# Kernel tuning notes

Measured on AMD Instinct MI355X. Metric: run time of the kernel, lower is better.

The kernel has to match this reference:

```python
import jax, jax.numpy as jnp
import numpy as np

EPS = 1e-5

def _batchnorm(x, gamma, beta):
    # training-mode BatchNorm1d: biased variance over the batch axis
    mean = jnp.mean(x, axis=0)
    var = jnp.mean(jnp.square(x - mean), axis=0)
    return (x - mean) * jax.lax.rsqrt(var + EPS) * gamma + beta

def setup_inputs() -> dict:
    key = jax.random.key(0)
    ks = jax.random.split(key, 20)
    N, E, T = 100000, 400000, 1000000
    ATOM, BOND, ANGLE = 128, 128, 64
    s = 0.05
    return {
        "vertex_feat": jax.random.normal(ks[0], (N, ATOM), jnp.float32),
        "edge_feat": jax.random.normal(ks[1], (E, BOND), jnp.float32),
        "angle_feat": jax.random.normal(ks[2], (T, ANGLE), jnp.float32),
        "edge_index": jax.random.randint(ks[3], (2, E), 0, N),
        "k_idx": jax.random.randint(ks[4], (T,), 0, E),   # b_i: bond indices
        "j_idx": jax.random.randint(ks[5], (T,), 0, N),   # a: center atom indices
        "i_idx": jax.random.randint(ks[6], (T,), 0, N),   # b_j: indexes vertex rows per source code
        "w_core_src": jax.random.normal(ks[7], (BOND, ATOM), jnp.float32) * s,
        "w_core_dst": jax.random.normal(ks[8], (BOND, ATOM), jnp.float32) * s,
        "w_core_bond": jax.random.normal(ks[9], (BOND, BOND), jnp.float32) * s,
        "w_core_angle": jax.random.normal(ks[10], (BOND, ANGLE), jnp.float32) * s,
        "w_gate_src": jax.random.normal(ks[11], (BOND, ATOM), jnp.float32) * s,
        "w_gate_dst": jax.random.normal(ks[12], (BOND, ATOM), jnp.float32) * s,
        "w_gate_bond": jax.random.normal(ks[13], (BOND, BOND), jnp.float32) * s,
        "w_gate_angle": jax.random.normal(ks[14], (BOND, ANGLE), jnp.float32) * s,
        "bn_core_gamma": jnp.ones((BOND,), jnp.float32),
        "bn_core_beta": jnp.zeros((BOND,), jnp.float32),
        "bn_gate_gamma": jnp.ones((BOND,), jnp.float32),
        "bn_gate_beta": jnp.zeros((BOND,), jnp.float32),
        "w_out": jax.random.normal(ks[15], (BOND, BOND), jnp.float32) * s,
    }

def _branch(vertex_feat, edge_feat, angle_feat, k_idx, j_idx, i_idx, ws, wd, wb, wa):
    # reverse_scatter chain == gather-add:
    # out[t] = (angle @ wa.T)[t] + (v @ ws.T)[j_idx[t]] + (e @ wb.T)[k_idx[t]] + (v @ wd.T)[i_idx[t]]
    center = vertex_feat @ ws.T            # [N, bond]
    bond_i = edge_feat @ wb.T              # [E, bond]
    bond_j = vertex_feat @ wd.T            # [N, bond]
    angles = angle_feat @ wa.T             # [T, bond]
    return angles + center[j_idx] + bond_i[k_idx] + bond_j[i_idx]

def reference(vertex_feat, edge_feat, angle_feat, edge_index, k_idx, j_idx, i_idx,
              w_core_src, w_core_dst, w_core_bond, w_core_angle,
              w_gate_src, w_gate_dst, w_gate_bond, w_gate_angle,
              bn_core_gamma, bn_core_beta, bn_gate_gamma, bn_gate_beta, w_out):
    E = edge_feat.shape[0]
    core = _branch(vertex_feat, edge_feat, angle_feat, k_idx, j_idx, i_idx,
                   w_core_src, w_core_dst, w_core_bond, w_core_angle)   # [T, bond]
    gate = _branch(vertex_feat, edge_feat, angle_feat, k_idx, j_idx, i_idx,
                   w_gate_src, w_gate_dst, w_gate_bond, w_gate_angle)   # [T, bond]
    core = jax.nn.silu(_batchnorm(core, bn_core_gamma, bn_core_beta))
    gate = jax.nn.sigmoid(_batchnorm(gate, bn_gate_gamma, bn_gate_beta))
    update = core * gate                                                # [T, bond]
    new_bond = jax.ops.segment_sum(update, k_idx, num_segments=E)       # [E, bond]
    new_bond = new_bond @ w_out.T
    return new_bond + edge_feat
```

## Files before the change

kernel.cpp:

```cpp
#include <hip/hip_runtime.h>
#include <hip/hip_bf16.h>

typedef unsigned short u16;
typedef unsigned int u32;
typedef __attribute__((ext_vector_type(8))) short bf8;
typedef __attribute__((ext_vector_type(4))) float f32x4;

__device__ __forceinline__ float bf2f(u16 u) {
    u32 v = ((u32)u) << 16;
    float f;
    __builtin_memcpy(&f, &v, 4);
    return f;
}
__device__ __forceinline__ u16 f2bf(float f) {
    u32 v;
    __builtin_memcpy(&v, &f, 4);
    u32 r = (v + 0x7fffu + ((v >> 16) & 1u)) >> 16;
    return (u16)r;
}
__device__ __forceinline__ u32 pk2(float a, float b) {
    return (u32)f2bf(a) | ((u32)f2bf(b) << 16);
}
__device__ __forceinline__ void unpack4(uint2 u, float* f) {
    f[0] = bf2f((u16)(u.x & 0xffffu));
    f[1] = bf2f((u16)(u.x >> 16));
    f[2] = bf2f((u16)(u.y & 0xffffu));
    f[3] = bf2f((u16)(u.y >> 16));
}

#define BM 128
#define BN 128
#define BK 64
#define LSTR 72

__global__ void detect_dtype(const u16* __restrict__ v, int* __restrict__ flag)
{
    __shared__ int red[256];
    int tid = threadIdx.x;
    int cnt = 0;
    for (int i = tid; i < 8192; i += 256) {
        u16 u = v[2 * i];
        int e = (u >> 7) & 0xFF;
        cnt += (e >= 160) ? 1 : 0;
    }
    red[tid] = cnt;
    __syncthreads();
    for (int s = 128; s > 0; s >>= 1) {
        if (tid < s) red[tid] += red[tid + s];
        __syncthreads();
    }
    if (tid == 0) flag[0] = (red[0] > 400) ? 1 : 0;
}

__global__ __launch_bounds__(256)
void gemm_bt(const void* __restrict__ Av, const u16* __restrict__ W,
             u16* __restrict__ C, const int* __restrict__ flag,
             int M, int K, int Ncols)
{
    __shared__ u16 As[BM][LSTR];
    __shared__ u16 Ws[BN][LSTR];
    const bool isf32 = flag[0] != 0;
    const int tid = threadIdx.x;
    const int m0 = blockIdx.x * BM;
    const int n0 = blockIdx.y * BN;
    const int wave = tid >> 6, lane = tid & 63;
    const int l16 = lane & 15, quad = lane >> 4;
    const int wrow = (wave >> 1) * 64, wcol = (wave & 1) * 64;

    f32x4 acc[4][4];
    for (int mi = 0; mi < 4; ++mi)
        for (int ni = 0; ni < 4; ++ni)
            for (int r = 0; r < 4; ++r) acc[mi][ni][r] = 0.f;

    for (int kk = 0; kk < K; kk += BK) {
        for (int it = 0; it < 4; ++it) {
            int c = tid + it * 256;
            int row = c >> 3, col8 = (c & 7) * 8;
            uint4 v = make_uint4(0, 0, 0, 0);
            int gr = m0 + row;
            if (gr < M) {
                if (!isf32) {
                    v = *(const uint4*)((const u16*)Av + (size_t)gr * K + (kk + col8));
                } else {
                    const float* Af = (const float*)Av + (size_t)gr * K + (kk + col8);
                    float4 x = *(const float4*)Af;
                    float4 y = *(const float4*)(Af + 4);
                    v = make_uint4(pk2(x.x, x.y), pk2(x.z, x.w), pk2(y.x, y.y), pk2(y.z, y.w));
                }
            }
            *(uint4*)(&As[row][col8]) = v;
        }
        for (int it = 0; it < 4; ++it) {
            int c = tid + it * 256;
            int row = c >> 3, col8 = (c & 7) * 8;
            uint4 v = *(const uint4*)(W + (size_t)(n0 + row) * K + (kk + col8));
            *(uint4*)(&Ws[row][col8]) = v;
        }
        __syncthreads();
        for (int ko = 0; ko < BK; ko += 32) {
            bf8 af[4], bw[4];
            for (int mi = 0; mi < 4; ++mi)
                af[mi] = *(const bf8*)(&As[wrow + mi * 16 + l16][ko + quad * 8]);
            for (int ni = 0; ni < 4; ++ni)
                bw[ni] = *(const bf8*)(&Ws[wcol + ni * 16 + l16][ko + quad * 8]);
            for (int mi = 0; mi < 4; ++mi)
                for (int ni = 0; ni < 4; ++ni)
                    acc[mi][ni] = __builtin_amdgcn_mfma_f32_16x16x32_bf16(
                        af[mi], bw[ni], acc[mi][ni], 0, 0, 0);
        }
        __syncthreads();
    }
    for (int mi = 0; mi < 4; ++mi) {
        int rbase = m0 + wrow + mi * 16 + quad * 4;
        for (int r = 0; r < 4; ++r) {
            int row = rbase + r;
            if (row >= M) continue;
            for (int ni = 0; ni < 4; ++ni) {
                int col = n0 + wcol + ni * 16 + l16;
                C[(size_t)row * Ncols + col] = f2bf(acc[mi][ni][r]);
            }
        }
    }
}

__global__ __launch_bounds__(256)
void gemm_out(const float* __restrict__ Aacc, const void* __restrict__ Wv_,
              const void* __restrict__ Edgev, void* __restrict__ Outv,
              const int* __restrict__ flag, int M)
{
    __shared__ u16 As[BM][LSTR];
    __shared__ u16 Ws[BN][LSTR];
    const bool isf32 = flag[0] != 0;
    const int tid = threadIdx.x;
    const int m0 = blockIdx.x * BM;
    const int wave = tid >> 6, lane = tid & 63;
    const int l16 = lane & 15, quad = lane >> 4;
    const int wrow = (wave >> 1) * 64, wcol = (wave & 1) * 64;

    f32x4 acc[4][4];
    for (int mi = 0; mi < 4; ++mi)
        for (int ni = 0; ni < 4; ++ni)
            for (int r = 0; r < 4; ++r) acc[mi][ni][r] = 0.f;

    for (int kk = 0; kk < 128; kk += BK) {
        for (int it = 0; it < 4; ++it) {
            int c = tid + it * 256;
            int row = c >> 3, col8 = (c & 7) * 8;
            int gr = m0 + row;
            uint4 v = make_uint4(0, 0, 0, 0);
            if (gr < M) {
                const float* src = Aacc + (size_t)gr * 128 + kk + col8;
                v = make_uint4(pk2(src[0], src[1]), pk2(src[2], src[3]),
                               pk2(src[4], src[5]), pk2(src[6], src[7]));
            }
            *(uint4*)(&As[row][col8]) = v;
        }
        for (int it = 0; it < 4; ++it) {
            int c = tid + it * 256;
            int row = c >> 3, col8 = (c & 7) * 8;
            uint4 v;
            if (!isf32) {
                v = *(const uint4*)((const u16*)Wv_ + (size_t)row * 128 + (kk + col8));
            } else {
                const float* Wf = (const float*)Wv_ + (size_t)row * 128 + (kk + col8);
                float4 x = *(const float4*)Wf;
                float4 y = *(const float4*)(Wf + 4);
                v = make_uint4(pk2(x.x, x.y), pk2(x.z, x.w), pk2(y.x, y.y), pk2(y.z, y.w));
            }
            *(uint4*)(&Ws[row][col8]) = v;
        }
        __syncthreads();
        for (int ko = 0; ko < BK; ko += 32) {
            bf8 af[4], bw[4];
            for (int mi = 0; mi < 4; ++mi)
                af[mi] = *(const bf8*)(&As[wrow + mi * 16 + l16][ko + quad * 8]);
            for (int ni = 0; ni < 4; ++ni)
                bw[ni] = *(const bf8*)(&Ws[wcol + ni * 16 + l16][ko + quad * 8]);
            for (int mi = 0; mi < 4; ++mi)
                for (int ni = 0; ni < 4; ++ni)
                    acc[mi][ni] = __builtin_amdgcn_mfma_f32_16x16x32_bf16(
                        af[mi], bw[ni], acc[mi][ni], 0, 0, 0);
        }
        __syncthreads();
    }
    for (int mi = 0; mi < 4; ++mi) {
        int rbase = m0 + wrow + mi * 16 + quad * 4;
        for (int r = 0; r < 4; ++r) {
            int row = rbase + r;
            if (row >= M) continue;
            for (int ni = 0; ni < 4; ++ni) {
                int col = wcol + ni * 16 + l16;
                size_t idx = (size_t)row * 128 + col;
                float e = isf32 ? ((const float*)Edgev)[idx] : bf2f(((const u16*)Edgev)[idx]);
                float v = acc[mi][ni][r] + e;
                if (isf32) ((float*)Outv)[idx] = v;
                else       ((u16*)Outv)[idx] = f2bf(v);
            }
        }
    }
}

__global__ __launch_bounds__(256)
void gather_stats(u16* __restrict__ CG, const u16* __restrict__ Vout,
                  const u16* __restrict__ Eout,
                  const int* __restrict__ jidx, const int* __restrict__ kidx,
                  const int* __restrict__ iidx, float* __restrict__ stats, int T)
{
    const int tid = threadIdx.x;
    const int q = tid & 63;
    const int wv = tid >> 6;
    const int p = q * 4;
    float sum[4] = {0.f, 0.f, 0.f, 0.f};
    float ssq[4] = {0.f, 0.f, 0.f, 0.f};
    for (long t = (long)blockIdx.x * 4 + wv; t < T; t += (long)gridDim.x * 4) {
        int j = jidx[t], k = kidx[t], i = iidx[t];
        uint2 ua = *(const uint2*)(CG + t * 256 + p);
        uint2 uj = *(const uint2*)(Vout + (size_t)j * 512 + p);
        uint2 uk = *(const uint2*)(Eout + (size_t)k * 256 + p);
        uint2 ui = *(const uint2*)(Vout + (size_t)i * 512 + 256 + p);
        float fa[4], fj[4], fk[4], fi[4];
        unpack4(ua, fa); unpack4(uj, fj); unpack4(uk, fk); unpack4(ui, fi);
        float v[4];
        for (int x = 0; x < 4; ++x) {
            v[x] = fa[x] + fj[x] + fk[x] + fi[x];
            sum[x] += v[x];
            ssq[x] += v[x] * v[x];
        }
        uint2 o;
        o.x = pk2(v[0], v[1]);
        o.y = pk2(v[2], v[3]);
        *(uint2*)(CG + t * 256 + p) = o;
    }
    __shared__ float red[512];
    red[tid] = 0.f;
    red[tid + 256] = 0.f;
    __syncthreads();
    for (int x = 0; x < 4; ++x) {
        atomicAdd(&red[p + x], sum[x]);
        atomicAdd(&red[256 + p + x], ssq[x]);
    }
    __syncthreads();
    atomicAdd(&stats[tid], red[tid]);
    atomicAdd(&stats[tid + 256], red[tid + 256]);
}

__global__ void bn_finalize(const float* __restrict__ stats,
                            const void* __restrict__ gc, const void* __restrict__ bc,
                            const void* __restrict__ gg, const void* __restrict__ bg,
                            float* __restrict__ ab, const int* __restrict__ flag,
                            float invT)
{
    const bool isf32 = flag[0] != 0;
    int p = threadIdx.x;
    float mean = stats[p] * invT;
    float var = stats[256 + p] * invT - mean * mean;
    const void* gsrc = (p < 128) ? gc : gg;
    const void* bsrc = (p < 128) ? bc : bg;
    int pi = p & 127;
    float g = isf32 ? ((const float*)gsrc)[pi] : bf2f(((const u16*)gsrc)[pi]);
    float b = isf32 ? ((const float*)bsrc)[pi] : bf2f(((const u16*)bsrc)[pi]);
    float a = g * rsqrtf(var + 1e-5f);
    ab[p] = a;
    ab[256 + p] = b - mean * a;
}


__global__ __launch_bounds__(256)
void hist_k(const int* __restrict__ kidx, int* __restrict__ cnt, int T)
{
    for (int t = blockIdx.x * 256 + threadIdx.x; t < T; t += gridDim.x * 256)
        atomicAdd(&cnt[kidx[t]], 1);
}

#define SCHUNK 2048

__global__ __launch_bounds__(256)
void scan_blocks(const int* __restrict__ cnt, int* __restrict__ bsum, int E)
{
    __shared__ int red[256];
    int b = blockIdx.x, t = threadIdx.x;
    int base = b * SCHUNK + t * 8;
    int s = 0;
    for (int i = 0; i < 8; ++i) {
        int idx = base + i;
        s += (idx < E) ? cnt[idx] : 0;
    }
    red[t] = s;
    __syncthreads();
    for (int st = 128; st > 0; st >>= 1) {
        if (t < st) red[t] += red[t + st];
        __syncthreads();
    }
    if (t == 0) bsum[b] = red[0];
}

__global__ void scan_partials(int* __restrict__ bsum, int NB,
                              int* __restrict__ offs, int E, int T)
{
    __shared__ int sh[256];
    int t = threadIdx.x;
    int v = (t < NB) ? bsum[t] : 0;
    sh[t] = v;
    __syncthreads();
    for (int d = 1; d < 256; d <<= 1) {
        int x = (t >= d) ? sh[t - d] : 0;
        __syncthreads();
        sh[t] += x;
        __syncthreads();
    }
    if (t < NB) bsum[t] = sh[t] - v;
    if (t == 0) offs[E] = T;
}

__global__ __launch_bounds__(256)
void scan_chunks(const int* __restrict__ cnt, const int* __restrict__ bsum,
                 int* __restrict__ offs, int E)
{
    __shared__ int sh[256];
    int b = blockIdx.x, t = threadIdx.x;
    int base = b * SCHUNK + t * 8;
    int loc[8];
    int s = 0;
    for (int i = 0; i < 8; ++i) {
        int idx = base + i;
        loc[i] = (idx < E) ? cnt[idx] : 0;
    }
    for (int i = 0; i < 8; ++i) { int v = loc[i]; loc[i] = s; s += v; }
    sh[t] = s;
    __syncthreads();
    for (int d = 1; d < 256; d <<= 1) {
        int x = (t >= d) ? sh[t - d] : 0;
        __syncthreads();
        sh[t] += x;
        __syncthreads();
    }
    int ex = sh[t] - s;
    int off = bsum[b] + ex;
    for (int i = 0; i < 8; ++i) {
        int idx = base + i;
        if (idx < E) offs[idx] = off + loc[i];
    }
}

__global__ __launch_bounds__(256)
void fill_k(const int* __restrict__ kidx, const int* __restrict__ offs,
            int* __restrict__ cur, int* __restrict__ blist, int T)
{
    for (int t = blockIdx.x * 256 + threadIdx.x; t < T; t += gridDim.x * 256) {
        int k = kidx[t];
        int pos = offs[k] + atomicAdd(&cur[k], 1);
        blist[pos] = t;
    }
}

__global__ __launch_bounds__(256)
void seg_update(const u16* __restrict__ CG, const float* __restrict__ ab,
                const int* __restrict__ offs, const int* __restrict__ blist,
                float* __restrict__ acc, int E)
{
    const int tid = threadIdx.x;
    const int q = tid & 63;
    const int wv = tid >> 6;
    const int f = q * 2;
    const float ac0 = ab[f], ac1 = ab[f + 1];
    const float ag0 = ab[128 + f], ag1 = ab[128 + f + 1];
    const float bc0 = ab[256 + f], bc1 = ab[256 + f + 1];
    const float bg0 = ab[384 + f], bg1 = ab[384 + f + 1];
    for (int e = blockIdx.x * 4 + wv; e < E; e += gridDim.x * 4) {
        int s = offs[e], en = offs[e + 1];
        float u0 = 0.f, u1 = 0.f;
        for (int idx = s; idx < en; ++idx) {
            int t = blist[idx];
            u32 c2 = *(const u32*)(CG + (size_t)t * 256 + f);
            u32 g2 = *(const u32*)(CG + (size_t)t * 256 + 128 + f);
            float c0 = bf2f((u16)(c2 & 0xffffu)) * ac0 + bc0;
            float c1 = bf2f((u16)(c2 >> 16)) * ac1 + bc1;
            float g0 = bf2f((u16)(g2 & 0xffffu)) * ag0 + bg0;
            float g1 = bf2f((u16)(g2 >> 16)) * ag1 + bg1;
            float s0 = 1.f / (1.f + __expf(-c0));
            float s1 = 1.f / (1.f + __expf(-c1));
            float t0 = 1.f / (1.f + __expf(-g0));
            float t1 = 1.f / (1.f + __expf(-g1));
            u0 += c0 * s0 * t0;
            u1 += c1 * s1 * t1;
        }
        *(float2*)(acc + (size_t)e * 128 + f) = make_float2(u0, u1);
    }
}

__device__ __forceinline__ u16 ld_bf(const void* p, size_t idx, bool isf32)
{
    return isf32 ? f2bf(((const float*)p)[idx]) : ((const u16*)p)[idx];
}

__global__ void pack_weights(const void* __restrict__ wcs, const void* __restrict__ wcd,
                             const void* __restrict__ wcb, const void* __restrict__ wca,
                             const void* __restrict__ wgs, const void* __restrict__ wgd,
                             const void* __restrict__ wgb, const void* __restrict__ wga,
                             u16* __restrict__ Wv, u16* __restrict__ We, u16* __restrict__ Wa,
                             const int* __restrict__ flag)
{
    const bool isf32 = flag[0] != 0;
    int tid = blockIdx.x * 256 + threadIdx.x;
    {
        int row = tid >> 7, col = tid & 127;
        const void* src = (row < 128) ? wcs : (row < 256) ? wgs : (row < 384) ? wcd : wgd;
        Wv[tid] = ld_bf(src, (size_t)(row & 127) * 128 + col, isf32);
    }
    if (tid < 256 * 128) {
        int row = tid >> 7, col = tid & 127;
        const void* src = (row < 128) ? wcb : wgb;
        We[tid] = ld_bf(src, (size_t)(row & 127) * 128 + col, isf32);
    }
    if (tid < 256 * 64) {
        int row = tid >> 6, col = tid & 63;
        const void* src = (row < 128) ? wca : wga;
        Wa[tid] = ld_bf(src, (size_t)(row & 127) * 64 + col, isf32);
    }
}

extern "C" void kernel_launch(void* const* d_in, const int* in_sizes, int n_in,
                              void* d_out, int out_size, void* d_ws, size_t ws_size,
                              hipStream_t stream)
{
    const void* vertex = d_in[0];
    const void* edge   = d_in[1];
    const void* angle  = d_in[2];
    const int* kidx = (const int*)d_in[4];
    const int* jidx = (const int*)d_in[5];
    const int* iidx = (const int*)d_in[6];

    const int N = in_sizes[0] / 128;
    const int E = in_sizes[1] / 128;
    const int T = in_sizes[2] / 64;

    char* p = (char*)d_ws;
    auto alloc = [&](size_t bytes) {
        char* r = p;
        p += (bytes + 255) & ~(size_t)255;
        return r;
    };
    u16* Wv = (u16*)alloc((size_t)512 * 128 * 2);
    u16* We = (u16*)alloc((size_t)256 * 128 * 2);
    u16* Wa = (u16*)alloc((size_t)256 * 64 * 2);
    float* stats = (float*)alloc(512 * 4);
    float* ab = (float*)alloc(512 * 4);
    int* flag = (int*)alloc(256);
    u16* Vout = (u16*)alloc((size_t)N * 512 * 2);
    u16* Eout = (u16*)alloc((size_t)E * 256 * 2);
    u16* CG   = (u16*)alloc((size_t)T * 256 * 2);
    float* acc = (float*)Vout;

    char* tail = (char*)acc + (size_t)E * 512;
    int* cnt   = (int*)tail;
    int* offs  = cnt + ((E + 63) & ~63);
    int* blist = offs + ((E + 1 + 63) & ~63);
    int* bsum  = blist + ((T + 63) & ~63);
    const int NB = (E + SCHUNK - 1) / SCHUNK;

    hipMemsetAsync(stats, 0, 512 * 4, stream);
    detect_dtype<<<1, 256, 0, stream>>>((const u16*)vertex, flag);
    pack_weights<<<256, 256, 0, stream>>>(d_in[7], d_in[8], d_in[9], d_in[10],
                                          d_in[11], d_in[12], d_in[13], d_in[14],
                                          Wv, We, Wa, flag);
    gemm_bt<<<dim3((N + 127) / 128, 4), 256, 0, stream>>>(vertex, Wv, Vout, flag, N, 128, 512);
    gemm_bt<<<dim3((E + 127) / 128, 2), 256, 0, stream>>>(edge, We, Eout, flag, E, 128, 256);
    gemm_bt<<<dim3((T + 127) / 128, 2), 256, 0, stream>>>(angle, Wa, CG, flag, T, 64, 256);
    gather_stats<<<2048, 256, 0, stream>>>(CG, Vout, Eout, jidx, kidx, iidx, stats, T);

    hipMemsetAsync(cnt, 0, (size_t)E * 4, stream);
    hist_k<<<2048, 256, 0, stream>>>(kidx, cnt, T);
    scan_blocks<<<NB, 256, 0, stream>>>(cnt, bsum, E);
    scan_partials<<<1, 256, 0, stream>>>(bsum, NB, offs, E, T);
    scan_chunks<<<NB, 256, 0, stream>>>(cnt, bsum, offs, E);
    hipMemsetAsync(cnt, 0, (size_t)E * 4, stream);
    fill_k<<<2048, 256, 0, stream>>>(kidx, offs, cnt, blist, T);

    bn_finalize<<<1, 256, 0, stream>>>(stats, d_in[15], d_in[16], d_in[17], d_in[18],
                                       ab, flag, 1.0f / (float)T);
    seg_update<<<2048, 256, 0, stream>>>(CG, ab, offs, blist, acc, E);
    gemm_out<<<dim3((E + 127) / 128, 1), 256, 0, stream>>>(acc, d_in[19], edge, d_out, flag, E);
}
```

Baseline: 1.902 ms.

## Fuse angle GEMM with gather-add and batch-norm statistics epilogue

Replaces the separate angle-feature GEMM and the gather_stats pass with a single kernel. Each tile's GEMM output is staged in shared memory, then the gathered vertex and edge projections are added, and per-channel sum and sum-of-squares are accumulated before CG is written once. This removes one full write and read of the T x 256 bf16 intermediate. Statistics now go into 64 partial slots to reduce atomic contention, and bn_finalize sums those slots. In exchange, each block's gather uses 2-element per-lane loads instead of 4, and the kernel uses more shared memory per block.

Result: no change. 1.909 ms (+0.4%).

```diff
diff --git a/kernel.cpp b/kernel.cpp
--- a/kernel.cpp
+++ b/kernel.cpp
@@ -124,6 +124,112 @@
 }
 
 __global__ __launch_bounds__(256)
+void gemm_angle_fused(const void* __restrict__ Av, const u16* __restrict__ Wa,
+                      const u16* __restrict__ Vout, const u16* __restrict__ Eout,
+                      const int* __restrict__ jidx, const int* __restrict__ kidx,
+                      const int* __restrict__ iidx,
+                      u16* __restrict__ CG, float* __restrict__ stats2,
+                      const int* __restrict__ flag, int T)
+{
+    __shared__ u16 sh[2 * BM * LSTR];
+    u16 (*As)[LSTR] = (u16(*)[LSTR])sh;
+    u16 (*Ws)[LSTR] = (u16(*)[LSTR])(sh + BM * LSTR);
+    const bool isf32 = flag[0] != 0;
+    const int tid = threadIdx.x;
+    const int m0 = blockIdx.x * BM;
+    const int h = blockIdx.y;
+    const int n0 = h * 128;
+    const int wave = tid >> 6, lane = tid & 63;
+    const int l16 = lane & 15, quad = lane >> 4;
+    const int wrow = (wave >> 1) * 64, wcol = (wave & 1) * 64;
+
+    f32x4 acc[4][4];
+    for (int mi = 0; mi < 4; ++mi)
+        for (int ni = 0; ni < 4; ++ni)
+            for (int r = 0; r < 4; ++r) acc[mi][ni][r] = 0.f;
+
+    for (int it = 0; it < 4; ++it) {
+        int c = tid + it * 256;
+        int row = c >> 3, col8 = (c & 7) * 8;
+        uint4 v = make_uint4(0, 0, 0, 0);
+        int gr = m0 + row;
+        if (gr < T) {
+            if (!isf32) {
+                v = *(const uint4*)((const u16*)Av + (size_t)gr * 64 + col8);
+            } else {
+                const float* Af = (const float*)Av + (size_t)gr * 64 + col8;
+                float4 x = *(const float4*)Af;
+                float4 y = *(const float4*)(Af + 4);
+                v = make_uint4(pk2(x.x, x.y), pk2(x.z, x.w), pk2(y.x, y.y), pk2(y.z, y.w));
+            }
+        }
+        *(uint4*)(&As[row][col8]) = v;
+    }
+    for (int it = 0; it < 4; ++it) {
+        int c = tid + it * 256;
+        int row = c >> 3, col8 = (c & 7) * 8;
+        uint4 v = *(const uint4*)(Wa + (size_t)(n0 + row) * 64 + col8);
+        *(uint4*)(&Ws[row][col8]) = v;
+    }
+    __syncthreads();
+    for (int ko = 0; ko < 64; ko += 32) {
+        bf8 af[4], bw[4];
+        for (int mi = 0; mi < 4; ++mi)
+            af[mi] = *(const bf8*)(&As[wrow + mi * 16 + l16][ko + quad * 8]);
+        for (int ni = 0; ni < 4; ++ni)
+            bw[ni] = *(const bf8*)(&Ws[wcol + ni * 16 + l16][ko + quad * 8]);
+        for (int mi = 0; mi < 4; ++mi)
+            for (int ni = 0; ni < 4; ++ni)
+                acc[mi][ni] = __builtin_amdgcn_mfma_f32_16x16x32_bf16(
+                    af[mi], bw[ni], acc[mi][ni], 0, 0, 0);
+    }
+    __syncthreads();
+
+    u16 (*Cs)[136] = (u16(*)[136])sh;
+    for (int mi = 0; mi < 4; ++mi) {
+        int rbase = wrow + mi * 16 + quad * 4;
+        for (int r = 0; r < 4; ++r)
+            for (int ni = 0; ni < 4; ++ni)
+                Cs[rbase + r][wcol + ni * 16 + l16] = f2bf(acc[mi][ni][r]);
+    }
+    __syncthreads();
+
+    const int q = lane;
+    const int p = q * 2;
+    float sum0 = 0.f, sum1 = 0.f, ssq0 = 0.f, ssq1 = 0.f;
+    for (int rr = wave; rr < 128; rr += 4) {
+        long t = (long)m0 + rr;
+        if (t >= T) break;
+        int j = jidx[t], k = kidx[t], i = iidx[t];
+        u32 ua = *(const u32*)(&Cs[rr][p]);
+        u32 uj = *(const u32*)(Vout + (size_t)j * 512 + n0 + p);
+        u32 uk = *(const u32*)(Eout + (size_t)k * 256 + n0 + p);
+        u32 ui = *(const u32*)(Vout + (size_t)i * 512 + 256 + n0 + p);
+        float v0 = bf2f((u16)(ua & 0xffffu)) + bf2f((u16)(uj & 0xffffu))
+                 + bf2f((u16)(uk & 0xffffu)) + bf2f((u16)(ui & 0xffffu));
+        float v1 = bf2f((u16)(ua >> 16)) + bf2f((u16)(uj >> 16))
+                 + bf2f((u16)(uk >> 16)) + bf2f((u16)(ui >> 16));
+        sum0 += v0; sum1 += v1;
+        ssq0 += v0 * v0; ssq1 += v1 * v1;
+        *(u32*)(CG + (size_t)t * 256 + n0 + p) = pk2(v0, v1);
+    }
+
+    __syncthreads();
+    float* red = (float*)sh;
+    red[wave * 128 + p] = sum0;
+    red[wave * 128 + p + 1] = sum1;
+    red[512 + wave * 128 + p] = ssq0;
+    red[512 + wave * 128 + p + 1] = ssq1;
+    __syncthreads();
+    {
+        int c = tid & 127, s = tid >> 7;
+        float v = red[s * 512 + c] + red[s * 512 + 128 + c]
+                + red[s * 512 + 256 + c] + red[s * 512 + 384 + c];
+        atomicAdd(&stats2[(size_t)(blockIdx.x & 63) * 512 + s * 256 + n0 + c], v);
+    }
+}
+
+__global__ __launch_bounds__(256)
 void gemm_out(const float* __restrict__ Aacc, const void* __restrict__ Wv_,
               const void* __restrict__ Edgev, void* __restrict__ Outv,
               const int* __restrict__ flag, int M)
@@ -200,51 +306,7 @@
     }
 }
 
-__global__ __launch_bounds__(256)
-void gather_stats(u16* __restrict__ CG, const u16* __restrict__ Vout,
-                  const u16* __restrict__ Eout,
-                  const int* __restrict__ jidx, const int* __restrict__ kidx,
-                  const int* __restrict__ iidx, float* __restrict__ stats, int T)
-{
-    const int tid = threadIdx.x;
-    const int q = tid & 63;
-    const int wv = tid >> 6;
-    const int p = q * 4;
-    float sum[4] = {0.f, 0.f, 0.f, 0.f};
-    float ssq[4] = {0.f, 0.f, 0.f, 0.f};
-    for (long t = (long)blockIdx.x * 4 + wv; t < T; t += (long)gridDim.x * 4) {
-        int j = jidx[t], k = kidx[t], i = iidx[t];
-        uint2 ua = *(const uint2*)(CG + t * 256 + p);
-        uint2 uj = *(const uint2*)(Vout + (size_t)j * 512 + p);
-        uint2 uk = *(const uint2*)(Eout + (size_t)k * 256 + p);
-        uint2 ui = *(const uint2*)(Vout + (size_t)i * 512 + 256 + p);
-        float fa[4], fj[4], fk[4], fi[4];
-        unpack4(ua, fa); unpack4(uj, fj); unpack4(uk, fk); unpack4(ui, fi);
-        float v[4];
-        for (int x = 0; x < 4; ++x) {
-            v[x] = fa[x] + fj[x] + fk[x] + fi[x];
-            sum[x] += v[x];
-            ssq[x] += v[x] * v[x];
-        }
-        uint2 o;
-        o.x = pk2(v[0], v[1]);
-        o.y = pk2(v[2], v[3]);
-        *(uint2*)(CG + t * 256 + p) = o;
-    }
-    __shared__ float red[512];
-    red[tid] = 0.f;
-    red[tid + 256] = 0.f;
-    __syncthreads();
-    for (int x = 0; x < 4; ++x) {
-        atomicAdd(&red[p + x], sum[x]);
-        atomicAdd(&red[256 + p + x], ssq[x]);
-    }
-    __syncthreads();
-    atomicAdd(&stats[tid], red[tid]);
-    atomicAdd(&stats[tid + 256], red[tid + 256]);
-}
-
-__global__ void bn_finalize(const float* __restrict__ stats,
+__global__ void bn_finalize(const float* __restrict__ stats2,
                             const void* __restrict__ gc, const void* __restrict__ bc,
                             const void* __restrict__ gg, const void* __restrict__ bg,
                             float* __restrict__ ab, const int* __restrict__ flag,
@@ -252,8 +314,13 @@
 {
     const bool isf32 = flag[0] != 0;
     int p = threadIdx.x;
-    float mean = stats[p] * invT;
-    float var = stats[256 + p] * invT - mean * mean;
+    float s = 0.f, q = 0.f;
+    for (int k = 0; k < 64; ++k) {
+        s += stats2[(size_t)k * 512 + p];
+        q += stats2[(size_t)k * 512 + 256 + p];
+    }
+    float mean = s * invT;
+    float var = q * invT - mean * mean;
     const void* gsrc = (p < 128) ? gc : gg;
     const void* bsrc = (p < 128) ? bc : bg;
     int pi = p & 127;
@@ -443,7 +510,7 @@
     u16* Wv = (u16*)alloc((size_t)512 * 128 * 2);
     u16* We = (u16*)alloc((size_t)256 * 128 * 2);
     u16* Wa = (u16*)alloc((size_t)256 * 64 * 2);
-    float* stats = (float*)alloc(512 * 4);
+    float* stats2 = (float*)alloc((size_t)64 * 512 * 4);
     float* ab = (float*)alloc(512 * 4);
     int* flag = (int*)alloc(256);
     u16* Vout = (u16*)alloc((size_t)N * 512 * 2);
@@ -458,15 +525,15 @@
     int* bsum  = blist + ((T + 63) & ~63);
     const int NB = (E + SCHUNK - 1) / SCHUNK;
 
-    hipMemsetAsync(stats, 0, 512 * 4, stream);
+    hipMemsetAsync(stats2, 0, (size_t)64 * 512 * 4, stream);
     detect_dtype<<<1, 256, 0, stream>>>((const u16*)vertex, flag);
     pack_weights<<<256, 256, 0, stream>>>(d_in[7], d_in[8], d_in[9], d_in[10],
                                           d_in[11], d_in[12], d_in[13], d_in[14],
                                           Wv, We, Wa, flag);
     gemm_bt<<<dim3((N + 127) / 128, 4), 256, 0, stream>>>(vertex, Wv, Vout, flag, N, 128, 512);
     gemm_bt<<<dim3((E + 127) / 128, 2), 256, 0, stream>>>(edge, We, Eout, flag, E, 128, 256);
-    gemm_bt<<<dim3((T + 127) / 128, 2), 256, 0, stream>>>(angle, Wa, CG, flag, T, 64, 256);
-    gather_stats<<<2048, 256, 0, stream>>>(CG, Vout, Eout, jidx, kidx, iidx, stats, T);
+    gemm_angle_fused<<<dim3((T + 127) / 128, 2), 256, 0, stream>>>(
+        angle, Wa, Vout, Eout, jidx, kidx, iidx, CG, stats2, flag, T);
 
     hipMemsetAsync(cnt, 0, (size_t)E * 4, stream);
     hist_k<<<2048, 256, 0, stream>>>(kidx, cnt, T);
@@ -476,7 +543,7 @@
     hipMemsetAsync(cnt, 0, (size_t)E * 4, stream);
     fill_k<<<2048, 256, 0, stream>>>(kidx, offs, cnt, blist, T);
 
-    bn_finalize<<<1, 256, 0, stream>>>(stats, d_in[15], d_in[16], d_in[17], d_in[18],
+    bn_finalize<<<1, 256, 0, stream>>>(stats2, d_in[15], d_in[16], d_in[17], d_in[18],
                                        ab, flag, 1.0f / (float)T);
     seg_update<<<2048, 256, 0, stream>>>(CG, ab, offs, blist, acc, E);
     gemm_out<<<dim3((E + 127) / 128, 1), 256, 0, stream>>>(acc, d_in[19], edge, d_out, flag, E);
```

## Fuse segment-sum update with output GEMM and swap GEMM grid axes

Applied to the files above, without the earlier changes.

Merges the segmented sum of the gated update and the final w_out projection into one kernel. Each block reduces 128 edge rows into shared memory as bf16, then runs MFMA against a pre-packed bf16 w_out read directly from global memory. This removes the fp32 intermediate accumulator round trip through HBM and one kernel launch. It also swaps the grid axes of gemm_bt so blocks sharing an A row-tile run adjacently, and adds nontemporal loads and stores on the streamed CG buffer. The cost is lower parallelism in the segment phase (fixed 32 rows per wave, one block per 128 edges) and an extra bf16 rounding of the summed update before the GEMM.

Result: slower. 2.015 ms (+5.9%).

```diff
diff --git a/kernel.cpp b/kernel.cpp
--- a/kernel.cpp
+++ b/kernel.cpp
@@ -4,6 +4,7 @@
 typedef unsigned short u16;
 typedef unsigned int u32;
 typedef __attribute__((ext_vector_type(8))) short bf8;
+typedef __attribute__((ext_vector_type(2))) unsigned int u32x2;
 typedef __attribute__((ext_vector_type(4))) float f32x4;
 
 __device__ __forceinline__ float bf2f(u16 u) {
@@ -20,12 +21,6 @@
 }
 __device__ __forceinline__ u32 pk2(float a, float b) {
     return (u32)f2bf(a) | ((u32)f2bf(b) << 16);
-}
-__device__ __forceinline__ void unpack4(uint2 u, float* f) {
-    f[0] = bf2f((u16)(u.x & 0xffffu));
-    f[1] = bf2f((u16)(u.x >> 16));
-    f[2] = bf2f((u16)(u.y & 0xffffu));
-    f[3] = bf2f((u16)(u.y >> 16));
 }
 
 #define BM 128
@@ -61,8 +56,8 @@
     __shared__ u16 Ws[BN][LSTR];
     const bool isf32 = flag[0] != 0;
     const int tid = threadIdx.x;
-    const int m0 = blockIdx.x * BM;
-    const int n0 = blockIdx.y * BN;
+    const int m0 = blockIdx.y * BM;
+    const int n0 = blockIdx.x * BN;
     const int wave = tid >> 6, lane = tid & 63;
     const int l16 = lane & 15, quad = lane >> 4;
     const int wrow = (wave >> 1) * 64, wcol = (wave & 1) * 64;
@@ -124,83 +119,6 @@
 }
 
 __global__ __launch_bounds__(256)
-void gemm_out(const float* __restrict__ Aacc, const void* __restrict__ Wv_,
-              const void* __restrict__ Edgev, void* __restrict__ Outv,
-              const int* __restrict__ flag, int M)
-{
-    __shared__ u16 As[BM][LSTR];
-    __shared__ u16 Ws[BN][LSTR];
-    const bool isf32 = flag[0] != 0;
-    const int tid = threadIdx.x;
-    const int m0 = blockIdx.x * BM;
-    const int wave = tid >> 6, lane = tid & 63;
-    const int l16 = lane & 15, quad = lane >> 4;
-    const int wrow = (wave >> 1) * 64, wcol = (wave & 1) * 64;
-
-    f32x4 acc[4][4];
-    for (int mi = 0; mi < 4; ++mi)
-        for (int ni = 0; ni < 4; ++ni)
-            for (int r = 0; r < 4; ++r) acc[mi][ni][r] = 0.f;
-
-    for (int kk = 0; kk < 128; kk += BK) {
-        for (int it = 0; it < 4; ++it) {
-            int c = tid + it * 256;
-            int row = c >> 3, col8 = (c & 7) * 8;
-            int gr = m0 + row;
-            uint4 v = make_uint4(0, 0, 0, 0);
-            if (gr < M) {
-                const float* src = Aacc + (size_t)gr * 128 + kk + col8;
-                v = make_uint4(pk2(src[0], src[1]), pk2(src[2], src[3]),
-                               pk2(src[4], src[5]), pk2(src[6], src[7]));
-            }
-            *(uint4*)(&As[row][col8]) = v;
-        }
-        for (int it = 0; it < 4; ++it) {
-            int c = tid + it * 256;
-            int row = c >> 3, col8 = (c & 7) * 8;
-            uint4 v;
-            if (!isf32) {
-                v = *(const uint4*)((const u16*)Wv_ + (size_t)row * 128 + (kk + col8));
-            } else {
-                const float* Wf = (const float*)Wv_ + (size_t)row * 128 + (kk + col8);
-                float4 x = *(const float4*)Wf;
-                float4 y = *(const float4*)(Wf + 4);
-                v = make_uint4(pk2(x.x, x.y), pk2(x.z, x.w), pk2(y.x, y.y), pk2(y.z, y.w));
-            }
-            *(uint4*)(&Ws[row][col8]) = v;
-        }
-        __syncthreads();
-        for (int ko = 0; ko < BK; ko += 32) {
-            bf8 af[4], bw[4];
-            for (int mi = 0; mi < 4; ++mi)
-                af[mi] = *(const bf8*)(&As[wrow + mi * 16 + l16][ko + quad * 8]);
-            for (int ni = 0; ni < 4; ++ni)
-                bw[ni] = *(const bf8*)(&Ws[wcol + ni * 16 + l16][ko + quad * 8]);
-            for (int mi = 0; mi < 4; ++mi)
-                for (int ni = 0; ni < 4; ++ni)
-                    acc[mi][ni] = __builtin_amdgcn_mfma_f32_16x16x32_bf16(
-                        af[mi], bw[ni], acc[mi][ni], 0, 0, 0);
-        }
-        __syncthreads();
-    }
-    for (int mi = 0; mi < 4; ++mi) {
-        int rbase = m0 + wrow + mi * 16 + quad * 4;
-        for (int r = 0; r < 4; ++r) {
-            int row = rbase + r;
-            if (row >= M) continue;
-            for (int ni = 0; ni < 4; ++ni) {
-                int col = wcol + ni * 16 + l16;
-                size_t idx = (size_t)row * 128 + col;
-                float e = isf32 ? ((const float*)Edgev)[idx] : bf2f(((const u16*)Edgev)[idx]);
-                float v = acc[mi][ni][r] + e;
-                if (isf32) ((float*)Outv)[idx] = v;
-                else       ((u16*)Outv)[idx] = f2bf(v);
-            }
-        }
-    }
-}
-
-__global__ __launch_bounds__(256)
 void gather_stats(u16* __restrict__ CG, const u16* __restrict__ Vout,
                   const u16* __restrict__ Eout,
                   const int* __restrict__ jidx, const int* __restrict__ kidx,
@@ -214,22 +132,27 @@
     float ssq[4] = {0.f, 0.f, 0.f, 0.f};
     for (long t = (long)blockIdx.x * 4 + wv; t < T; t += (long)gridDim.x * 4) {
         int j = jidx[t], k = kidx[t], i = iidx[t];
-        uint2 ua = *(const uint2*)(CG + t * 256 + p);
+        u32x2 ua = __builtin_nontemporal_load((const u32x2*)(CG + t * 256 + p));
         uint2 uj = *(const uint2*)(Vout + (size_t)j * 512 + p);
         uint2 uk = *(const uint2*)(Eout + (size_t)k * 256 + p);
         uint2 ui = *(const uint2*)(Vout + (size_t)i * 512 + 256 + p);
-        float fa[4], fj[4], fk[4], fi[4];
-        unpack4(ua, fa); unpack4(uj, fj); unpack4(uk, fk); unpack4(ui, fi);
         float v[4];
+        v[0] = bf2f((u16)(ua[0] & 0xffffu)) + bf2f((u16)(uj.x & 0xffffu))
+             + bf2f((u16)(uk.x & 0xffffu)) + bf2f((u16)(ui.x & 0xffffu));
+        v[1] = bf2f((u16)(ua[0] >> 16)) + bf2f((u16)(uj.x >> 16))
+             + bf2f((u16)(uk.x >> 16)) + bf2f((u16)(ui.x >> 16));
+        v[2] = bf2f((u16)(ua[1] & 0xffffu)) + bf2f((u16)(uj.y & 0xffffu))
+             + bf2f((u16)(uk.y & 0xffffu)) + bf2f((u16)(ui.y & 0xffffu));
+        v[3] = bf2f((u16)(ua[1] >> 16)) + bf2f((u16)(uj.y >> 16))
+             + bf2f((u16)(uk.y >> 16)) + bf2f((u16)(ui.y >> 16));
         for (int x = 0; x < 4; ++x) {
-            v[x] = fa[x] + fj[x] + fk[x] + fi[x];
             sum[x] += v[x];
             ssq[x] += v[x] * v[x];
         }
-        uint2 o;
-        o.x = pk2(v[0], v[1]);
-        o.y = pk2(v[2], v[3]);
-        *(uint2*)(CG + t * 256 + p) = o;
+        u32x2 o;
+        o[0] = pk2(v[0], v[1]);
+        o[1] = pk2(v[2], v[3]);
+        __builtin_nontemporal_store(o, (u32x2*)(CG + t * 256 + p));
     }
     __shared__ float red[512];
     red[tid] = 0.f;
@@ -354,37 +277,86 @@
 }
 
 __global__ __launch_bounds__(256)
-void seg_update(const u16* __restrict__ CG, const float* __restrict__ ab,
-                const int* __restrict__ offs, const int* __restrict__ blist,
-                float* __restrict__ acc, int E)
-{
+void seg_gemm_out(const u16* __restrict__ CG, const float* __restrict__ ab,
+                  const int* __restrict__ offs, const int* __restrict__ blist,
+                  const u16* __restrict__ Wo, const void* __restrict__ Edgev,
+                  void* __restrict__ Outv, const int* __restrict__ flag, int E)
+{
+    __shared__ u16 As[128][136];
+    const bool isf32 = flag[0] != 0;
     const int tid = threadIdx.x;
-    const int q = tid & 63;
-    const int wv = tid >> 6;
-    const int f = q * 2;
-    const float ac0 = ab[f], ac1 = ab[f + 1];
-    const float ag0 = ab[128 + f], ag1 = ab[128 + f + 1];
-    const float bc0 = ab[256 + f], bc1 = ab[256 + f + 1];
-    const float bg0 = ab[384 + f], bg1 = ab[384 + f + 1];
-    for (int e = blockIdx.x * 4 + wv; e < E; e += gridDim.x * 4) {
-        int s = offs[e], en = offs[e + 1];
-        float u0 = 0.f, u1 = 0.f;
-        for (int idx = s; idx < en; ++idx) {
-            int t = blist[idx];
-            u32 c2 = *(const u32*)(CG + (size_t)t * 256 + f);
-            u32 g2 = *(const u32*)(CG + (size_t)t * 256 + 128 + f);
-            float c0 = bf2f((u16)(c2 & 0xffffu)) * ac0 + bc0;
-            float c1 = bf2f((u16)(c2 >> 16)) * ac1 + bc1;
-            float g0 = bf2f((u16)(g2 & 0xffffu)) * ag0 + bg0;
-            float g1 = bf2f((u16)(g2 >> 16)) * ag1 + bg1;
-            float s0 = 1.f / (1.f + __expf(-c0));
-            float s1 = 1.f / (1.f + __expf(-c1));
-            float t0 = 1.f / (1.f + __expf(-g0));
-            float t1 = 1.f / (1.f + __expf(-g1));
-            u0 += c0 * s0 * t0;
-            u1 += c1 * s1 * t1;
-        }
-        *(float2*)(acc + (size_t)e * 128 + f) = make_float2(u0, u1);
+    const int wave = tid >> 6, lane = tid & 63;
+    const int m0 = blockIdx.x * 128;
+    const int f = lane * 2;
+
+    {
+        const float ac0 = ab[f], ac1 = ab[f + 1];
+        const float ag0 = ab[128 + f], ag1 = ab[128 + f + 1];
+        const float bc0 = ab[256 + f], bc1 = ab[256 + f + 1];
+        const float bg0 = ab[384 + f], bg1 = ab[384 + f + 1];
+        for (int i = 0; i < 32; ++i) {
+            int rl = wave * 32 + i;
+            int e = m0 + rl;
+            float u0 = 0.f, u1 = 0.f;
+            if (e < E) {
+                int s = offs[e], en = offs[e + 1];
+                for (int idx = s; idx < en; ++idx) {
+                    int t = blist[idx];
+                    u32 c2 = __builtin_nontemporal_load(
+                        (const u32*)(CG + (size_t)t * 256 + f));
+                    u32 g2 = __builtin_nontemporal_load(
+                        (const u32*)(CG + (size_t)t * 256 + 128 + f));
+                    float c0 = bf2f((u16)(c2 & 0xffffu)) * ac0 + bc0;
+                    float c1 = bf2f((u16)(c2 >> 16)) * ac1 + bc1;
+                    float g0 = bf2f((u16)(g2 & 0xffffu)) * ag0 + bg0;
+                    float g1 = bf2f((u16)(g2 >> 16)) * ag1 + bg1;
+                    float s0 = 1.f / (1.f + __expf(-c0));
+                    float s1 = 1.f / (1.f + __expf(-c1));
+                    float t0 = 1.f / (1.f + __expf(-g0));
+                    float t1 = 1.f / (1.f + __expf(-g1));
+                    u0 += c0 * s0 * t0;
+                    u1 += c1 * s1 * t1;
+                }
+            }
+            *(u32*)(&As[rl][f]) = pk2(u0, u1);
+        }
+    }
+    __syncthreads();
+
+    const int l16 = lane & 15, quad = lane >> 4;
+    const int wrow = (wave >> 1) * 64, wcol = (wave & 1) * 64;
+    f32x4 acc[4][4];
+    for (int mi = 0; mi < 4; ++mi)
+        for (int ni = 0; ni < 4; ++ni)
+            for (int r = 0; r < 4; ++r) acc[mi][ni][r] = 0.f;
+
+    for (int kk = 0; kk < 128; kk += 32) {
+        bf8 af[4], bw[4];
+        for (int mi = 0; mi < 4; ++mi)
+            af[mi] = *(const bf8*)(&As[wrow + mi * 16 + l16][kk + quad * 8]);
+        for (int ni = 0; ni < 4; ++ni)
+            bw[ni] = *(const bf8*)(Wo + (size_t)(wcol + ni * 16 + l16) * 128
+                                       + kk + quad * 8);
+        for (int mi = 0; mi < 4; ++mi)
+            for (int ni = 0; ni < 4; ++ni)
+                acc[mi][ni] = __builtin_amdgcn_mfma_f32_16x16x32_bf16(
+                    af[mi], bw[ni], acc[mi][ni], 0, 0, 0);
+    }
+
+    for (int mi = 0; mi < 4; ++mi) {
+        int rbase = m0 + wrow + mi * 16 + quad * 4;
+        for (int r = 0; r < 4; ++r) {
+            int row = rbase + r;
+            if (row >= E) continue;
+            for (int ni = 0; ni < 4; ++ni) {
+                int col = wcol + ni * 16 + l16;
+                size_t idx = (size_t)row * 128 + col;
+                float e = isf32 ? ((const float*)Edgev)[idx] : bf2f(((const u16*)Edgev)[idx]);
+                float v = acc[mi][ni][r] + e;
+                if (isf32) ((float*)Outv)[idx] = v;
+                else       ((u16*)Outv)[idx] = f2bf(v);
+            }
+        }
     }
 }
 
@@ -397,7 +369,9 @@
                              const void* __restrict__ wcb, const void* __restrict__ wca,
                              const void* __restrict__ wgs, const void* __restrict__ wgd,
                              const void* __restrict__ wgb, const void* __restrict__ wga,
-                             u16* __restrict__ Wv, u16* __restrict__ We, u16* __restrict__ Wa,
+                             const void* __restrict__ wout,
+                             u16* __restrict__ Wv, u16* __restrict__ We,
+                             u16* __restrict__ Wa, u16* __restrict__ Wo,
                              const int* __restrict__ flag)
 {
     const bool isf32 = flag[0] != 0;
@@ -416,6 +390,9 @@
         int row = tid >> 6, col = tid & 63;
         const void* src = (row < 128) ? wca : wga;
         Wa[tid] = ld_bf(src, (size_t)(row & 127) * 64 + col, isf32);
+    }
+    if (tid < 128 * 128) {
+        Wo[tid] = ld_bf(wout, (size_t)tid, isf32);
     }
 }
 
@@ -443,16 +420,15 @@
     u16* Wv = (u16*)alloc((size_t)512 * 128 * 2);
     u16* We = (u16*)alloc((size_t)256 * 128 * 2);
     u16* Wa = (u16*)alloc((size_t)256 * 64 * 2);
+    u16* Wo = (u16*)alloc((size_t)128 * 128 * 2);
     float* stats = (float*)alloc(512 * 4);
     float* ab = (float*)alloc(512 * 4);
     int* flag = (int*)alloc(256);
     u16* Vout = (u16*)alloc((size_t)N * 512 * 2);
     u16* Eout = (u16*)alloc((size_t)E * 256 * 2);
     u16* CG   = (u16*)alloc((size_t)T * 256 * 2);
-    float* acc = (float*)Vout;
-
-    char* tail = (char*)acc + (size_t)E * 512;
-    int* cnt   = (int*)tail;
+
+    int* cnt   = (int*)Vout;
     int* offs  = cnt + ((E + 63) & ~63);
     int* blist = offs + ((E + 1 + 63) & ~63);
     int* bsum  = blist + ((T + 63) & ~63);
@@ -462,10 +438,10 @@
     detect_dtype<<<1, 256, 0, stream>>>((const u16*)vertex, flag);
     pack_weights<<<256, 256, 0, stream>>>(d_in[7], d_in[8], d_in[9], d_in[10],
                                           d_in[11], d_in[12], d_in[13], d_in[14],
-                                          Wv, We, Wa, flag);
-    gemm_bt<<<dim3((N + 127) / 128, 4), 256, 0, stream>>>(vertex, Wv, Vout, flag, N, 128, 512);
-    gemm_bt<<<dim3((E + 127) / 128, 2), 256, 0, stream>>>(edge, We, Eout, flag, E, 128, 256);
-    gemm_bt<<<dim3((T + 127) / 128, 2), 256, 0, stream>>>(angle, Wa, CG, flag, T, 64, 256);
+                                          d_in[19], Wv, We, Wa, Wo, flag);
+    gemm_bt<<<dim3(4, (N + 127) / 128), 256, 0, stream>>>(vertex, Wv, Vout, flag, N, 128, 512);
+    gemm_bt<<<dim3(2, (E + 127) / 128), 256, 0, stream>>>(edge, We, Eout, flag, E, 128, 256);
+    gemm_bt<<<dim3(2, (T + 127) / 128), 256, 0, stream>>>(angle, Wa, CG, flag, T, 64, 256);
     gather_stats<<<2048, 256, 0, stream>>>(CG, Vout, Eout, jidx, kidx, iidx, stats, T);
 
     hipMemsetAsync(cnt, 0, (size_t)E * 4, stream);
@@ -478,6 +454,6 @@
 
     bn_finalize<<<1, 256, 0, stream>>>(stats, d_in[15], d_in[16], d_in[17], d_in[18],
                                        ab, flag, 1.0f / (float)T);
-    seg_update<<<2048, 256, 0, stream>>>(CG, ab, offs, blist, acc, E);
-    gemm_out<<<dim3((E + 127) / 128, 1), 256, 0, stream>>>(acc, d_in[19], edge, d_out, flag, E);
-}
+    seg_gemm_out<<<(E + 127) / 128, 256, 0, stream>>>(CG, ab, offs, blist, Wo,
+                                                      edge, d_out, flag, E);
+}
```
